# Kernel optimization log

Hardware: AMD Instinct MI355X
Metric: run time of the kernel (lower is better)

## Reference

```python
import math
import jax, jax.numpy as jnp
import numpy as np


def _sinkhorn_attn(q, n):
    """Log-domain Sinkhorn-Knopp, eps=1, max_iter=1, uniform marginals.
    cost C = -q @ q^T, so M = (-C + u + v)/eps = S + u + v with S = q q^T.
    Returns transport plan pi = exp(S + u_i + v_j).  q: [B, n, d]."""
    S = jnp.einsum('bnd,bmd->bnm', q, q)            # [B, n, n]
    log_marg = -math.log(n)                          # log(1/n)
    u = log_marg - jax.nn.logsumexp(S, axis=-1)      # [B, n] row update
    v = log_marg - jax.nn.logsumexp(S + u[..., :, None], axis=-2)  # [B, n] col update
    return jnp.exp(S + u[..., :, None] + v[..., None, :])


def reference(x, row_embed, col_embed):
    # x: [B, d, H, W]; row_embed/col_embed: [len_embedding, d//2]
    B, d, H, W = x.shape
    # learned positional embedding: [H, W, d] -> [d, H, W]
    x_emb = col_embed[:W]                             # [W, F]
    y_emb = row_embed[:H]                             # [H, F]
    F = x_emb.shape[-1]
    pos = jnp.concatenate([
        jnp.broadcast_to(x_emb[None, :, :], (H, W, F)),
        jnp.broadcast_to(y_emb[:, None, :], (H, W, F)),
    ], axis=-1).transpose(2, 0, 1)                    # [d, H, W]
    x = x + pos[None]

    n = H * W
    xf = x.reshape(B, d, n).transpose(0, 2, 1)        # [B, n, d] = q = k = v (v unscaled)
    inv_sqrtV = 1.0 / math.sqrt(math.sqrt(d))         # d**-0.25 applied to q and k each
    attn = _sinkhorn_attn(xf * inv_sqrtV, n)          # [B, n, n]
    out = jnp.einsum('bnm,bmd->bnd', attn, xf)        # [B, n, d]
    return out.transpose(0, 2, 1).reshape(B, d, H, W)


def setup_inputs() -> dict:
    key = jax.random.key(0)
    k1, k2, k3 = jax.random.split(key, 3)
    B, d, H, W = 32, 512, 32, 32
    len_emb, F = 32, d // 2
    return {
        'x': jax.random.normal(k1, (B, d, H, W), dtype=jnp.float32),
        'row_embed': jax.random.uniform(k2, (len_emb, F), dtype=jnp.float32),
        'col_embed': jax.random.uniform(k3, (len_emb, F), dtype=jnp.float32),
    }
```

## Files before the change

### kernel.cpp

```cpp
#include <hip/hip_runtime.h>
#include <hip/hip_fp16.h>
#include <math.h>

typedef _Float16 f16;
typedef _Float16 f16x8 __attribute__((ext_vector_type(8)));
typedef _Float16 f16x4 __attribute__((ext_vector_type(4)));
typedef float f32x4 __attribute__((ext_vector_type(4)));

namespace {
constexpr int kB = 32, kD = 512, kN = 1024, kF = 256;
constexpr float kScale = 0.04419417382415922f;
constexpr float kLogMarg = -6.931471805599453f;
constexpr float kMarg = 1.f / 1024.f;
constexpr float kPScale = 16384.f;
constexpr float kPInv = 1.f / 16384.f;
}

__device__ __forceinline__ void gload16(const void* g, void* l) {
  __builtin_amdgcn_global_load_lds(
      (const __attribute__((address_space(1))) void*)g,
      (__attribute__((address_space(3))) void*)l, 16, 0, 0);
}

__global__ __launch_bounds__(256) void k_prep(
    const float* __restrict__ x, const float* __restrict__ re,
    const float* __restrict__ ce, f16* __restrict__ xf,
    f16* __restrict__ xfT, int b0) {
  __shared__ f16 T[64][68];
  const int lb = blockIdx.z;
  const int i0 = blockIdx.x * 64, c0 = blockIdx.y * 64;
  const int t = threadIdx.x;
  const int il = (t & 15) * 4;
  const int cl = t >> 4;
  const size_t xbase = ((size_t)(b0 + lb) * kD) * kN;
#pragma unroll
  for (int p = 0; p < 4; p++) {
    const int c = c0 + cl + 16 * p;
    const int i = i0 + il;
    const float4 xv = *(const float4*)(x + xbase + (size_t)c * kN + i);
    float4 pv;
    if (c < kF) {
      pv.x = ce[((i + 0) & 31) * kF + c];
      pv.y = ce[((i + 1) & 31) * kF + c];
      pv.z = ce[((i + 2) & 31) * kF + c];
      pv.w = ce[((i + 3) & 31) * kF + c];
    } else {
      const float r = re[(i >> 5) * kF + (c - kF)];
      pv.x = r; pv.y = r; pv.z = r; pv.w = r;
    }
    const f16 h0 = (f16)(xv.x + pv.x), h1 = (f16)(xv.y + pv.y);
    const f16 h2 = (f16)(xv.z + pv.z), h3 = (f16)(xv.w + pv.w);
    f16* dT = xfT + ((size_t)lb * kD + c) * kN + i;
    *(f16x4*)dT = (f16x4){h0, h1, h2, h3};
    T[cl + 16 * p][il + 0] = h0; T[cl + 16 * p][il + 1] = h1;
    T[cl + 16 * p][il + 2] = h2; T[cl + 16 * p][il + 3] = h3;
  }
  __syncthreads();
#pragma unroll
  for (int p = 0; p < 4; p++) {
    const int ir = cl + 16 * p;
    const int cc = il;
    const f16 h0 = T[cc + 0][ir], h1 = T[cc + 1][ir];
    const f16 h2 = T[cc + 2][ir], h3 = T[cc + 3][ir];
    f16* dF = xf + ((size_t)lb * kN + i0 + ir) * kD + c0 + cc;
    *(f16x4*)dF = (f16x4){h0, h1, h2, h3};
  }
}

__global__ __launch_bounds__(256) void k_gemm_s(
    const f16* __restrict__ xf, f16* __restrict__ S16,
    float* __restrict__ rp) {
  __shared__ char sm[32768];
  const int lb = blockIdx.z;
  const int i0 = blockIdx.y * 128, j0 = blockIdx.x * 128;
  const char* base = (const char*)(xf + (size_t)lb * kN * kD);
  const int t = threadIdx.x;
  const int w = t >> 6, lane = t & 63;
  const int m_off = (w >> 1) * 64, n_off = (w & 1) * 64;
  const int quad = lane >> 4, l15 = lane & 15;
  const int swz = (l15 & 7) << 4;

  int srcA[4], srcB[4], ldsw[4];
#pragma unroll
  for (int p = 0; p < 4; p++) {
    const int off = p * 4096 + w * 1024 + lane * 16;
    const int r = off >> 7;
    const int cb = (off & 127) ^ ((r & 7) << 4);
    srcA[p] = (i0 + r) * (kD * 2) + cb;
    srcB[p] = (j0 + r) * (kD * 2) + cb;
    ldsw[p] = p * 4096 + w * 1024;
  }

  f32x4 acc[4][4];
#pragma unroll
  for (int a = 0; a < 4; a++)
#pragma unroll
    for (int b = 0; b < 4; b++) acc[a][b] = (f32x4){0.f, 0.f, 0.f, 0.f};

  for (int k0b = 0; k0b < kD * 2; k0b += 128) {
#pragma unroll
    for (int p = 0; p < 4; p++)
      gload16(base + srcA[p] + k0b, sm + ldsw[p]);
#pragma unroll
    for (int p = 0; p < 4; p++)
      gload16(base + srcB[p] + k0b, sm + 16384 + ldsw[p]);
    __syncthreads();
#pragma unroll
    for (int kk = 0; kk < 2; kk++) {
      f16x8 af[4], bf[4];
#pragma unroll
      for (int q = 0; q < 4; q++)
        af[q] = *(const f16x8*)(sm + (m_off + 16 * q + l15) * 128 +
                                ((kk * 64 + quad * 16) ^ swz));
#pragma unroll
      for (int q = 0; q < 4; q++)
        bf[q] = *(const f16x8*)(sm + 16384 + (n_off + 16 * q + l15) * 128 +
                                ((kk * 64 + quad * 16) ^ swz));
#pragma unroll
      for (int qa = 0; qa < 4; qa++)
#pragma unroll
        for (int qb = 0; qb < 4; qb++)
          acc[qa][qb] = __builtin_amdgcn_mfma_f32_16x16x32_f16(
              af[qa], bf[qb], acc[qa][qb], 0, 0, 0);
    }
    __syncthreads();
  }

  f16* Sb = S16 + (size_t)lb * kN * kN;
  const int jt2 = blockIdx.x * 2 + (w & 1);
  float* rpb = rp + ((size_t)lb * 16 + jt2) * kN + i0 + m_off;
#pragma unroll
  for (int qa = 0; qa < 4; qa++) {
    const int i = i0 + m_off + 16 * qa + quad * 4;
    float rs[4] = {0.f, 0.f, 0.f, 0.f};
#pragma unroll
    for (int qb = 0; qb < 4; qb++) {
      const int j = j0 + n_off + 16 * qb + l15;
#pragma unroll
      for (int r = 0; r < 4; r++) {
        const f16 h = (f16)(acc[qa][qb][r] * kScale);
        Sb[(size_t)(i + r) * kN + j] = h;
        rs[r] += __expf((float)h);
      }
    }
#pragma unroll
    for (int r = 0; r < 4; r++) {
      float s = rs[r];
      s += __shfl_xor(s, 1);
      s += __shfl_xor(s, 2);
      s += __shfl_xor(s, 4);
      s += __shfl_xor(s, 8);
      if (l15 == 0) rpb[16 * qa + 4 * quad + r] = s;
    }
  }
}

__global__ __launch_bounds__(256) void k_u(
    const float* __restrict__ rp, float* __restrict__ u) {
  const int lb = blockIdx.y;
  const int i = blockIdx.x * 256 + threadIdx.x;
  const float* r = rp + (size_t)lb * 16 * kN + i;
  float s = 0.f;
#pragma unroll
  for (int t = 0; t < 16; t++) s += r[(size_t)t * kN];
  u[lb * kN + i] = kLogMarg - __logf(s);
}

__global__ __launch_bounds__(256) void k_cs(
    const f16* __restrict__ S16, const float* __restrict__ u,
    float* __restrict__ cp) {
  const int lb = blockIdx.z;
  const int seg = blockIdx.y;
  const int j = blockIdx.x * 256 + threadIdx.x;
  const f16* Sb = S16 + (size_t)lb * kN * kN + j;
  const float* ub = u + lb * kN + seg * 64;
  const size_t rbase = (size_t)(seg * 64) * kN;
  float s = 0.f;
#pragma unroll 4
  for (int r = 0; r < 64; r++)
    s += __expf((float)Sb[rbase + (size_t)r * kN] + ub[r]);
  cp[((size_t)lb * 16 + seg) * kN + j] = s;
}

__global__ __launch_bounds__(256) void k_v(
    const float* __restrict__ cp, float* __restrict__ ev) {
  const int lb = blockIdx.y;
  const int j = blockIdx.x * 256 + threadIdx.x;
  const float* c = cp + (size_t)lb * 16 * kN + j;
  float s = 0.f;
#pragma unroll
  for (int r = 0; r < 16; r++) s += c[(size_t)r * kN];
  ev[lb * kN + j] = kMarg / s;
}

__global__ __launch_bounds__(256) void k_pt(
    const f16* __restrict__ S16, const float* __restrict__ u,
    const float* __restrict__ ev, f16* __restrict__ t16) {
  const int row = blockIdx.x;
  const float ui = u[row];
  const f16* Sr = S16 + (size_t)row * kN;
  const float* evb = ev + (size_t)(row >> 10) * kN;
  f16* Tr = t16 + (size_t)row * kN;
  const int j = threadIdx.x * 4;
  const f16x4 s = *(const f16x4*)(Sr + j);
  const float4 e = *(const float4*)(evb + j);
  f16x4 o;
  o[0] = (f16)(__expf((float)s[0] + ui) * e.x * kPScale);
  o[1] = (f16)(__expf((float)s[1] + ui) * e.y * kPScale);
  o[2] = (f16)(__expf((float)s[2] + ui) * e.z * kPScale);
  o[3] = (f16)(__expf((float)s[3] + ui) * e.w * kPScale);
  *(f16x4*)(Tr + j) = o;
}

__global__ __launch_bounds__(256) void k_gemm_o(
    const f16* __restrict__ xfT, const f16* __restrict__ P,
    float* __restrict__ out, int b0) {
  __shared__ char sm[32768];
  const int lb = blockIdx.z;
  const int i0 = blockIdx.x * 128, c0 = blockIdx.y * 128;
  const char* Ab = (const char*)(xfT + (size_t)lb * kD * kN);
  const char* Bb = (const char*)(P + (size_t)lb * kN * kN);
  const int t = threadIdx.x;
  const int w = t >> 6, lane = t & 63;
  const int m_off = (w >> 1) * 64, n_off = (w & 1) * 64;
  const int quad = lane >> 4, l15 = lane & 15;
  const int swz = (l15 & 7) << 4;

  int srcA[4], srcB[4], ldsw[4];
#pragma unroll
  for (int p = 0; p < 4; p++) {
    const int off = p * 4096 + w * 1024 + lane * 16;
    const int r = off >> 7;
    const int cb = (off & 127) ^ ((r & 7) << 4);
    srcA[p] = (c0 + r) * (kN * 2) + cb;
    srcB[p] = (i0 + r) * (kN * 2) + cb;
    ldsw[p] = p * 4096 + w * 1024;
  }

  f32x4 acc[4][4];
#pragma unroll
  for (int a = 0; a < 4; a++)
#pragma unroll
    for (int b = 0; b < 4; b++) acc[a][b] = (f32x4){0.f, 0.f, 0.f, 0.f};

  for (int k0b = 0; k0b < kN * 2; k0b += 128) {
#pragma unroll
    for (int p = 0; p < 4; p++)
      gload16(Ab + srcA[p] + k0b, sm + ldsw[p]);
#pragma unroll
    for (int p = 0; p < 4; p++)
      gload16(Bb + srcB[p] + k0b, sm + 16384 + ldsw[p]);
    __syncthreads();
#pragma unroll
    for (int kk = 0; kk < 2; kk++) {
      f16x8 af[4], bf[4];
#pragma unroll
      for (int q = 0; q < 4; q++)
        af[q] = *(const f16x8*)(sm + (m_off + 16 * q + l15) * 128 +
                                ((kk * 64 + quad * 16) ^ swz));
#pragma unroll
      for (int q = 0; q < 4; q++)
        bf[q] = *(const f16x8*)(sm + 16384 + (n_off + 16 * q + l15) * 128 +
                                ((kk * 64 + quad * 16) ^ swz));
#pragma unroll
      for (int qa = 0; qa < 4; qa++)
#pragma unroll
        for (int qb = 0; qb < 4; qb++)
          acc[qa][qb] = __builtin_amdgcn_mfma_f32_16x16x32_f16(
              af[qa], bf[qb], acc[qa][qb], 0, 0, 0);
    }
    __syncthreads();
  }

  float* ob = out + ((size_t)(b0 + lb) * kD) * kN;
#pragma unroll
  for (int qa = 0; qa < 4; qa++) {
    const int c = c0 + m_off + 16 * qa + quad * 4;
#pragma unroll
    for (int qb = 0; qb < 4; qb++) {
      const int i = i0 + n_off + 16 * qb + l15;
#pragma unroll
      for (int r = 0; r < 4; r++)
        ob[(size_t)(c + r) * kN + i] = acc[qa][qb][r] * kPInv;
    }
  }
}

extern "C" void kernel_launch(void* const* d_in, const int* in_sizes, int n_in,
                              void* d_out, int out_size, void* d_ws, size_t ws_size,
                              hipStream_t stream) {
  const float* x = (const float*)d_in[0];
  const float* re = (const float*)d_in[1];
  const float* ce = (const float*)d_in[2];
  float* out = (float*)d_out;

  char* wsb = (char*)d_ws;
  const size_t perb = 2097152ull + 1048576 + 1048576 + 2097152 +
                      4096 + 4096 + 65536 + 65536;
  int G = (int)(ws_size / perb);
  if (G >= 32) G = 32;
  else if (G >= 16) G = 16;
  else if (G >= 8) G = 8;
  else if (G >= 4) G = 4;
  else if (G < 1) G = 1;
  f16* S16 = (f16*)wsb;
  f16* xf = (f16*)(wsb + (size_t)G * 2097152);
  f16* xfT = (f16*)((char*)xf + (size_t)G * 1048576);
  f16* t16 = (f16*)((char*)xfT + (size_t)G * 1048576);
  float* u = (float*)((char*)t16 + (size_t)G * 2097152);
  float* ev = u + (size_t)G * kN;
  float* rp = ev + (size_t)G * kN;
  float* cp = rp + (size_t)G * 16 * kN;

  for (int b0 = 0; b0 < kB; b0 += G) {
    const int g = (kB - b0 < G) ? (kB - b0) : G;
    k_prep<<<dim3(16, 8, g), 256, 0, stream>>>(x, re, ce, xf, xfT, b0);
    k_gemm_s<<<dim3(8, 8, g), 256, 0, stream>>>(xf, S16, rp);
    k_u<<<dim3(4, g), 256, 0, stream>>>(rp, u);
    k_cs<<<dim3(4, 16, g), 256, 0, stream>>>(S16, u, cp);
    k_v<<<dim3(4, g), 256, 0, stream>>>(cp, ev);
    k_pt<<<g * kN, 256, 0, stream>>>(S16, u, ev, t16);
    k_gemm_o<<<dim3(8, 4, g), 256, 0, stream>>>(xfT, t16, out, b0);
  }
}
```

Before: 280.5 us.

## Double-buffer LDS tiles and remap workgroups across XCDs in both GEMMs

Both GEMM kernels now keep two LDS buffers (64KB), so the next K-tile is fetched into one buffer while MFMAs run on the other, replacing the load-sync-compute-sync loop. Workgroup IDs are also remapped so that consecutive tiles of the same batch go to the same XCD, aiming for better L2 reuse of the shared operand rows. The cost is double the LDS per block, which can lower occupancy. The grid dimensions are hardcoded in the remap.

Measured after the change: 256.1 us. -8.7%, faster.

```diff
diff --git a/kernel.cpp b/kernel.cpp
--- a/kernel.cpp
+++ b/kernel.cpp
@@ -70,9 +70,15 @@
 __global__ __launch_bounds__(256) void k_gemm_s(
     const f16* __restrict__ xf, f16* __restrict__ S16,
     float* __restrict__ rp) {
-  __shared__ char sm[32768];
-  const int lb = blockIdx.z;
-  const int i0 = blockIdx.y * 128, j0 = blockIdx.x * 128;
+  __shared__ char sm[65536];
+  const int nwg = (int)(gridDim.x * gridDim.y * gridDim.z);
+  const int lin = (int)(blockIdx.x +
+                        gridDim.x * (blockIdx.y + gridDim.y * blockIdx.z));
+  const int wid = (lin & 7) * (nwg >> 3) + (lin >> 3);
+  const int bx = wid & 7, by = (wid >> 3) & 7, bz = wid >> 6;
+
+  const int lb = bz;
+  const int i0 = by * 128, j0 = bx * 128;
   const char* base = (const char*)(xf + (size_t)lb * kN * kD);
   const int t = threadIdx.x;
   const int w = t >> 6, lane = t & 63;
@@ -97,24 +103,36 @@
 #pragma unroll
     for (int b = 0; b < 4; b++) acc[a][b] = (f32x4){0.f, 0.f, 0.f, 0.f};
 
-  for (int k0b = 0; k0b < kD * 2; k0b += 128) {
-#pragma unroll
-    for (int p = 0; p < 4; p++)
-      gload16(base + srcA[p] + k0b, sm + ldsw[p]);
-#pragma unroll
-    for (int p = 0; p < 4; p++)
-      gload16(base + srcB[p] + k0b, sm + 16384 + ldsw[p]);
-    __syncthreads();
+#pragma unroll
+  for (int p = 0; p < 4; p++) gload16(base + srcA[p], sm + ldsw[p]);
+#pragma unroll
+  for (int p = 0; p < 4; p++) gload16(base + srcB[p], sm + 16384 + ldsw[p]);
+  __syncthreads();
+
+#pragma unroll
+  for (int tt = 0; tt < 8; tt++) {
+    const int cur = tt & 1, nxt = cur ^ 1;
+    if (tt + 1 < 8) {
+      const int k0b = (tt + 1) * 128;
+#pragma unroll
+      for (int p = 0; p < 4; p++)
+        gload16(base + srcA[p] + k0b, sm + (nxt << 15) + ldsw[p]);
+#pragma unroll
+      for (int p = 0; p < 4; p++)
+        gload16(base + srcB[p] + k0b, sm + (nxt << 15) + 16384 + ldsw[p]);
+    }
+    const char* bA = sm + (cur << 15);
+    const char* bB = bA + 16384;
 #pragma unroll
     for (int kk = 0; kk < 2; kk++) {
       f16x8 af[4], bf[4];
 #pragma unroll
       for (int q = 0; q < 4; q++)
-        af[q] = *(const f16x8*)(sm + (m_off + 16 * q + l15) * 128 +
+        af[q] = *(const f16x8*)(bA + (m_off + 16 * q + l15) * 128 +
                                 ((kk * 64 + quad * 16) ^ swz));
 #pragma unroll
       for (int q = 0; q < 4; q++)
-        bf[q] = *(const f16x8*)(sm + 16384 + (n_off + 16 * q + l15) * 128 +
+        bf[q] = *(const f16x8*)(bB + (n_off + 16 * q + l15) * 128 +
                                 ((kk * 64 + quad * 16) ^ swz));
 #pragma unroll
       for (int qa = 0; qa < 4; qa++)
@@ -127,7 +145,7 @@
   }
 
   f16* Sb = S16 + (size_t)lb * kN * kN;
-  const int jt2 = blockIdx.x * 2 + (w & 1);
+  const int jt2 = bx * 2 + (w & 1);
   float* rpb = rp + ((size_t)lb * 16 + jt2) * kN + i0 + m_off;
 #pragma unroll
   for (int qa = 0; qa < 4; qa++) {
@@ -215,9 +233,15 @@
 __global__ __launch_bounds__(256) void k_gemm_o(
     const f16* __restrict__ xfT, const f16* __restrict__ P,
     float* __restrict__ out, int b0) {
-  __shared__ char sm[32768];
-  const int lb = blockIdx.z;
-  const int i0 = blockIdx.x * 128, c0 = blockIdx.y * 128;
+  __shared__ char sm[65536];
+  const int nwg = (int)(gridDim.x * gridDim.y * gridDim.z);
+  const int lin = (int)(blockIdx.x +
+                        gridDim.x * (blockIdx.y + gridDim.y * blockIdx.z));
+  const int wid = (lin & 7) * (nwg >> 3) + (lin >> 3);
+  const int bx = wid & 7, by = (wid >> 3) & 3, bz = wid >> 5;
+
+  const int lb = bz;
+  const int i0 = bx * 128, c0 = by * 128;
   const char* Ab = (const char*)(xfT + (size_t)lb * kD * kN);
   const char* Bb = (const char*)(P + (size_t)lb * kN * kN);
   const int t = threadIdx.x;
@@ -243,24 +267,36 @@
 #pragma unroll
     for (int b = 0; b < 4; b++) acc[a][b] = (f32x4){0.f, 0.f, 0.f, 0.f};
 
-  for (int k0b = 0; k0b < kN * 2; k0b += 128) {
-#pragma unroll
-    for (int p = 0; p < 4; p++)
-      gload16(Ab + srcA[p] + k0b, sm + ldsw[p]);
-#pragma unroll
-    for (int p = 0; p < 4; p++)
-      gload16(Bb + srcB[p] + k0b, sm + 16384 + ldsw[p]);
-    __syncthreads();
+#pragma unroll
+  for (int p = 0; p < 4; p++) gload16(Ab + srcA[p], sm + ldsw[p]);
+#pragma unroll
+  for (int p = 0; p < 4; p++) gload16(Bb + srcB[p], sm + 16384 + ldsw[p]);
+  __syncthreads();
+
+#pragma unroll
+  for (int tt = 0; tt < 16; tt++) {
+    const int cur = tt & 1, nxt = cur ^ 1;
+    if (tt + 1 < 16) {
+      const int k0b = (tt + 1) * 128;
+#pragma unroll
+      for (int p = 0; p < 4; p++)
+        gload16(Ab + srcA[p] + k0b, sm + (nxt << 15) + ldsw[p]);
+#pragma unroll
+      for (int p = 0; p < 4; p++)
+        gload16(Bb + srcB[p] + k0b, sm + (nxt << 15) + 16384 + ldsw[p]);
+    }
+    const char* bA = sm + (cur << 15);
+    const char* bB = bA + 16384;
 #pragma unroll
     for (int kk = 0; kk < 2; kk++) {
       f16x8 af[4], bf[4];
 #pragma unroll
       for (int q = 0; q < 4; q++)
-        af[q] = *(const f16x8*)(sm + (m_off + 16 * q + l15) * 128 +
+        af[q] = *(const f16x8*)(bA + (m_off + 16 * q + l15) * 128 +
                                 ((kk * 64 + quad * 16) ^ swz));
 #pragma unroll
       for (int q = 0; q < 4; q++)
-        bf[q] = *(const f16x8*)(sm + 16384 + (n_off + 16 * q + l15) * 128 +
+        bf[q] = *(const f16x8*)(bB + (n_off + 16 * q + l15) * 128 +
                                 ((kk * 64 + quad * 16) ^ swz));
 #pragma unroll
       for (int qa = 0; qa < 4; qa++)
```

## Rework both GEMMs into 256x256 tiles with double-buffered LDS pipeline

Applied to the files above, without the earlier changes.

Both MFMA GEMM kernels move from 128x128 tiles with 256 threads to 256x256 tiles with 512 threads and 128KB of LDS. The K loop now double-buffers A and B in LDS, issuing global-to-LDS loads for later K steps while MFMAs run, and uses explicit vmcnt waits, barriers and setprio around MFMA phases. Workgroup IDs are remapped across the grid to improve L2 locality. This targets exposed load latency and per-block overhead, in exchange for fewer workgroups (lower occupancy, fewer blocks for small batch groups) and more complex hand-tuned synchronization.

Result: faster. 239.0 us (-14.8%).

```diff
diff --git a/kernel.cpp b/kernel.cpp
--- a/kernel.cpp
+++ b/kernel.cpp
@@ -67,70 +67,141 @@
   }
 }
 
-__global__ __launch_bounds__(256) void k_gemm_s(
+#define AF_READ(q)                                                          \
+  _Pragma("unroll")                                                         \
+  for (int pa = 0; pa < 2; pa++)                                            \
+    _Pragma("unroll")                                                       \
+    for (int kk = 0; kk < 2; kk++)                                          \
+      af[pa][kk] = *(const f16x8*)(bA + (m_off + 32*(q) + 16*pa + l15)*128  \
+                                   + ((kk*64 + quad*16) ^ swz));
+
+#define MFMA_PH(q)                                                          \
+  __builtin_amdgcn_s_setprio(1);                                            \
+  _Pragma("unroll")                                                         \
+  for (int pa = 0; pa < 2; pa++)                                            \
+    _Pragma("unroll")                                                       \
+    for (int qb = 0; qb < 4; qb++)                                          \
+      _Pragma("unroll")                                                     \
+      for (int kk = 0; kk < 2; kk++)                                        \
+        acc[2*(q)+pa][qb] = __builtin_amdgcn_mfma_f32_16x16x32_f16(         \
+            af[pa][kk], bf[qb][kk], acc[2*(q)+pa][qb], 0, 0, 0);            \
+  __builtin_amdgcn_s_setprio(0);
+
+#define GEMM_KLOOP(NT, Abase, Bbase, sA, sB)                                \
+  _Pragma("unroll")                                                         \
+  for (int tt = 0; tt < (NT); tt++) {                                       \
+    const int cur = tt & 1, nxt = cur ^ 1;                                  \
+    const char* bA = sm + cur * 32768;                                      \
+    const char* bB = sm + 65536 + cur * 32768;                              \
+    char* wA = sm + nxt * 32768;                                            \
+    char* wB = sm + 65536 + cur * 32768;                                    \
+    const int kA = (tt + 1) * 128, kBB = (tt + 2) * 128;                    \
+    f16x8 bf[4][2], af[2][2];                                               \
+              \
+    _Pragma("unroll")                                                       \
+    for (int qb = 0; qb < 4; qb++)                                          \
+      _Pragma("unroll")                                                     \
+      for (int kk = 0; kk < 2; kk++)                                        \
+        bf[qb][kk] = *(const f16x8*)(bB + (n_off + 16*qb + l15)*128         \
+                                     + ((kk*64 + quad*16) ^ swz));          \
+    AF_READ(0)                                                              \
+    asm volatile("s_waitcnt lgkmcnt(0)" ::: "memory");                      \
+    __builtin_amdgcn_sched_barrier(0);                                      \
+    __builtin_amdgcn_s_barrier();                                           \
+    MFMA_PH(0)                                                              \
+                                         \
+    if (tt + 1 < (NT)) {                                                    \
+      gload16((Abase) + (sA)[0] + kA, wA + ldsw[0]);                        \
+      gload16((Abase) + (sA)[2] + kA, wA + ldsw[2]);                        \
+    }                                                                       \
+    AF_READ(1)                                                              \
+    __builtin_amdgcn_s_barrier();                                           \
+    MFMA_PH(1)                                                              \
+    if (tt == (NT) - 1) { asm volatile("s_waitcnt vmcnt(0)" ::: "memory"); }\
+    else                { asm volatile("s_waitcnt vmcnt(6)" ::: "memory"); }\
+    __builtin_amdgcn_s_barrier();                                           \
+    __builtin_amdgcn_sched_barrier(0);                                      \
+                                                                    \
+    AF_READ(2)                                                              \
+    __builtin_amdgcn_s_barrier();                                           \
+    MFMA_PH(2)                                                              \
+                        \
+    if (tt + 1 < (NT)) {                                                    \
+      gload16((Abase) + (sA)[1] + kA, wA + ldsw[1]);                        \
+      gload16((Abase) + (sA)[3] + kA, wA + ldsw[3]);                        \
+    }                                                                       \
+    if (tt + 2 < (NT)) {                                                    \
+      _Pragma("unroll")                                                     \
+      for (int p = 0; p < 4; p++)                                           \
+        gload16((Bbase) + (sB)[p] + kBB, wB + ldsw[p]);                     \
+    }                                                                       \
+    AF_READ(3)                                                              \
+    __builtin_amdgcn_s_barrier();                                           \
+    MFMA_PH(3)                                                              \
+    if (tt + 2 < (NT))      { asm volatile("s_waitcnt vmcnt(6)" ::: "memory"); } \
+    else if (tt + 1 < (NT)) { asm volatile("s_waitcnt vmcnt(2)" ::: "memory"); } \
+    __builtin_amdgcn_s_barrier();                                           \
+    __builtin_amdgcn_sched_barrier(0);                                      \
+  }
+
+#define GEMM_PROLOGUE(Abase, Bbase, sA, sB)                                 \
+  _Pragma("unroll")                                                         \
+  for (int p = 0; p < 4; p++) gload16((Bbase) + (sB)[p], sm + 65536 + ldsw[p]); \
+  gload16((Abase) + (sA)[0], sm + ldsw[0]);                                 \
+  gload16((Abase) + (sA)[2], sm + ldsw[2]);                                 \
+  gload16((Abase) + (sA)[1], sm + ldsw[1]);                                 \
+  gload16((Abase) + (sA)[3], sm + ldsw[3]);                                 \
+  _Pragma("unroll")                                                         \
+  for (int p = 0; p < 4; p++)                                               \
+    gload16((Bbase) + (sB)[p] + 128, sm + 65536 + 32768 + ldsw[p]);         \
+  f32x4 acc[8][4];                                                          \
+  _Pragma("unroll")                                                         \
+  for (int a = 0; a < 8; a++)                                               \
+    _Pragma("unroll")                                                       \
+    for (int b = 0; b < 4; b++) acc[a][b] = (f32x4){0.f, 0.f, 0.f, 0.f};    \
+  asm volatile("s_waitcnt vmcnt(6)" ::: "memory");                          \
+  __builtin_amdgcn_s_barrier();                                             \
+  __builtin_amdgcn_sched_barrier(0);
+
+__global__ __launch_bounds__(512) void k_gemm_s(
     const f16* __restrict__ xf, f16* __restrict__ S16,
     float* __restrict__ rp) {
-  __shared__ char sm[32768];
-  const int lb = blockIdx.z;
-  const int i0 = blockIdx.y * 128, j0 = blockIdx.x * 128;
+  __shared__ char sm[131072];
+  const int nwg = (int)(gridDim.x * gridDim.y * gridDim.z);
+  const int lin = (int)(blockIdx.x +
+                        gridDim.x * (blockIdx.y + gridDim.y * blockIdx.z));
+  const int wid = (lin & 7) * (nwg >> 3) + (lin >> 3);
+  const int bx = wid & 3, by = (wid >> 2) & 3, bz = wid >> 4;
+
+  const int lb = bz;
+  const int i0 = by * 256, j0 = bx * 256;
   const char* base = (const char*)(xf + (size_t)lb * kN * kD);
   const int t = threadIdx.x;
   const int w = t >> 6, lane = t & 63;
-  const int m_off = (w >> 1) * 64, n_off = (w & 1) * 64;
+  const int wm = w >> 2, wn = w & 3;
+  const int m_off = wm * 128, n_off = wn * 64;
   const int quad = lane >> 4, l15 = lane & 15;
   const int swz = (l15 & 7) << 4;
 
   int srcA[4], srcB[4], ldsw[4];
 #pragma unroll
   for (int p = 0; p < 4; p++) {
-    const int off = p * 4096 + w * 1024 + lane * 16;
+    const int off = p * 8192 + t * 16;
     const int r = off >> 7;
     const int cb = (off & 127) ^ ((r & 7) << 4);
     srcA[p] = (i0 + r) * (kD * 2) + cb;
     srcB[p] = (j0 + r) * (kD * 2) + cb;
-    ldsw[p] = p * 4096 + w * 1024;
-  }
-
-  f32x4 acc[4][4];
-#pragma unroll
-  for (int a = 0; a < 4; a++)
-#pragma unroll
-    for (int b = 0; b < 4; b++) acc[a][b] = (f32x4){0.f, 0.f, 0.f, 0.f};
-
-  for (int k0b = 0; k0b < kD * 2; k0b += 128) {
-#pragma unroll
-    for (int p = 0; p < 4; p++)
-      gload16(base + srcA[p] + k0b, sm + ldsw[p]);
-#pragma unroll
-    for (int p = 0; p < 4; p++)
-      gload16(base + srcB[p] + k0b, sm + 16384 + ldsw[p]);
-    __syncthreads();
-#pragma unroll
-    for (int kk = 0; kk < 2; kk++) {
-      f16x8 af[4], bf[4];
-#pragma unroll
-      for (int q = 0; q < 4; q++)
-        af[q] = *(const f16x8*)(sm + (m_off + 16 * q + l15) * 128 +
-                                ((kk * 64 + quad * 16) ^ swz));
-#pragma unroll
-      for (int q = 0; q < 4; q++)
-        bf[q] = *(const f16x8*)(sm + 16384 + (n_off + 16 * q + l15) * 128 +
-                                ((kk * 64 + quad * 16) ^ swz));
-#pragma unroll
-      for (int qa = 0; qa < 4; qa++)
-#pragma unroll
-        for (int qb = 0; qb < 4; qb++)
-          acc[qa][qb] = __builtin_amdgcn_mfma_f32_16x16x32_f16(
-              af[qa], bf[qb], acc[qa][qb], 0, 0, 0);
-    }
-    __syncthreads();
-  }
+    ldsw[p] = p * 8192 + w * 1024;
+  }
+
+  GEMM_PROLOGUE(base, base, srcA, srcB)
+  GEMM_KLOOP(8, base, base, srcA, srcB)
 
   f16* Sb = S16 + (size_t)lb * kN * kN;
-  const int jt2 = blockIdx.x * 2 + (w & 1);
-  float* rpb = rp + ((size_t)lb * 16 + jt2) * kN + i0 + m_off;
-#pragma unroll
-  for (int qa = 0; qa < 4; qa++) {
+  const int jt = bx * 4 + wn;
+  float* rpb = rp + ((size_t)lb * 16 + jt) * kN + i0 + m_off;
+#pragma unroll
+  for (int qa = 0; qa < 8; qa++) {
     const int i = i0 + m_off + 16 * qa + quad * 4;
     float rs[4] = {0.f, 0.f, 0.f, 0.f};
 #pragma unroll
@@ -212,69 +283,44 @@
   *(f16x4*)(Tr + j) = o;
 }
 
-__global__ __launch_bounds__(256) void k_gemm_o(
+__global__ __launch_bounds__(512) void k_gemm_o(
     const f16* __restrict__ xfT, const f16* __restrict__ P,
     float* __restrict__ out, int b0) {
-  __shared__ char sm[32768];
-  const int lb = blockIdx.z;
-  const int i0 = blockIdx.x * 128, c0 = blockIdx.y * 128;
+  __shared__ char sm[131072];
+  const int nwg = (int)(gridDim.x * gridDim.y * gridDim.z);
+  const int lin = (int)(blockIdx.x +
+                        gridDim.x * (blockIdx.y + gridDim.y * blockIdx.z));
+  const int wid = (lin & 7) * (nwg >> 3) + (lin >> 3);
+  const int bx = wid & 3, by = (wid >> 2) & 1, bz = wid >> 3;
+
+  const int lb = bz;
+  const int i0 = bx * 256, c0 = by * 256;
   const char* Ab = (const char*)(xfT + (size_t)lb * kD * kN);
   const char* Bb = (const char*)(P + (size_t)lb * kN * kN);
   const int t = threadIdx.x;
   const int w = t >> 6, lane = t & 63;
-  const int m_off = (w >> 1) * 64, n_off = (w & 1) * 64;
+  const int wm = w >> 2, wn = w & 3;
+  const int m_off = wm * 128, n_off = wn * 64;
   const int quad = lane >> 4, l15 = lane & 15;
   const int swz = (l15 & 7) << 4;
 
   int srcA[4], srcB[4], ldsw[4];
 #pragma unroll
   for (int p = 0; p < 4; p++) {
-    const int off = p * 4096 + w * 1024 + lane * 16;
+    const int off = p * 8192 + t * 16;
     const int r = off >> 7;
     const int cb = (off & 127) ^ ((r & 7) << 4);
     srcA[p] = (c0 + r) * (kN * 2) + cb;
     srcB[p] = (i0 + r) * (kN * 2) + cb;
-    ldsw[p] = p * 4096 + w * 1024;
-  }
-
-  f32x4 acc[4][4];
-#pragma unroll
-  for (int a = 0; a < 4; a++)
-#pragma unroll
-    for (int b = 0; b < 4; b++) acc[a][b] = (f32x4){0.f, 0.f, 0.f, 0.f};
-
-  for (int k0b = 0; k0b < kN * 2; k0b += 128) {
-#pragma unroll
-    for (int p = 0; p < 4; p++)
-      gload16(Ab + srcA[p] + k0b, sm + ldsw[p]);
-#pragma unroll
-    for (int p = 0; p < 4; p++)
-      gload16(Bb + srcB[p] + k0b, sm + 16384 + ldsw[p]);
-    __syncthreads();
-#pragma unroll
-    for (int kk = 0; kk < 2; kk++) {
-      f16x8 af[4], bf[4];
-#pragma unroll
-      for (int q = 0; q < 4; q++)
-        af[q] = *(const f16x8*)(sm + (m_off + 16 * q + l15) * 128 +
-                                ((kk * 64 + quad * 16) ^ swz));
-#pragma unroll
-      for (int q = 0; q < 4; q++)
-        bf[q] = *(const f16x8*)(sm + 16384 + (n_off + 16 * q + l15) * 128 +
-                                ((kk * 64 + quad * 16) ^ swz));
-#pragma unroll
-      for (int qa = 0; qa < 4; qa++)
-#pragma unroll
-        for (int qb = 0; qb < 4; qb++)
-          acc[qa][qb] = __builtin_amdgcn_mfma_f32_16x16x32_f16(
-              af[qa], bf[qb], acc[qa][qb], 0, 0, 0);
-    }
-    __syncthreads();
-  }
+    ldsw[p] = p * 8192 + w * 1024;
+  }
+
+  GEMM_PROLOGUE(Ab, Bb, srcA, srcB)
+  GEMM_KLOOP(16, Ab, Bb, srcA, srcB)
 
   float* ob = out + ((size_t)(b0 + lb) * kD) * kN;
 #pragma unroll
-  for (int qa = 0; qa < 4; qa++) {
+  for (int qa = 0; qa < 8; qa++) {
     const int c = c0 + m_off + 16 * qa + quad * 4;
 #pragma unroll
     for (int qb = 0; qb < 4; qb++) {
@@ -315,11 +361,11 @@
   for (int b0 = 0; b0 < kB; b0 += G) {
     const int g = (kB - b0 < G) ? (kB - b0) : G;
     k_prep<<<dim3(16, 8, g), 256, 0, stream>>>(x, re, ce, xf, xfT, b0);
-    k_gemm_s<<<dim3(8, 8, g), 256, 0, stream>>>(xf, S16, rp);
+    k_gemm_s<<<dim3(4, 4, g), 512, 0, stream>>>(xf, S16, rp);
     k_u<<<dim3(4, g), 256, 0, stream>>>(rp, u);
     k_cs<<<dim3(4, 16, g), 256, 0, stream>>>(S16, u, cp);
     k_v<<<dim3(4, g), 256, 0, stream>>>(cp, ev);
     k_pt<<<g * kN, 256, 0, stream>>>(S16, u, ev, t16);
-    k_gemm_o<<<dim3(8, 4, g), 256, 0, stream>>>(xfT, t16, out, b0);
-  }
-}
+    k_gemm_o<<<dim3(4, 2, g), 512, 0, stream>>>(xfT, t16, out, b0);
+  }
+}
```
